# Kernel tuning notes

Hardware: AMD Instinct MI355X
Metric: run time of the kernel (lower is better)

## Reference

```python
import jax, jax.numpy as jnp
import numpy as np

NUM_CAPS = 8
IN_CH = 768
OUT_CH = 64  # == num_routes
BATCH = 16384


def setup_inputs() -> dict:
    key = jax.random.key(0)
    ks = jax.random.split(key, 9)
    lim = 1.0 / np.sqrt(IN_CH)  # torch Linear default init range
    inp = {
        'img_emb': jax.random.normal(ks[0], (BATCH, IN_CH), jnp.float32),
        'capt_emb': jax.random.normal(ks[1], (BATCH, IN_CH), jnp.float32),
        'dct_emb': jax.random.normal(ks[2], (BATCH, IN_CH), jnp.float32),
        'W_img': jax.random.uniform(ks[3], (NUM_CAPS, OUT_CH, IN_CH), jnp.float32, -lim, lim),
        'b_img': jax.random.uniform(ks[4], (NUM_CAPS, OUT_CH), jnp.float32, -lim, lim),
        'W_capt': jax.random.uniform(ks[5], (NUM_CAPS, OUT_CH, IN_CH), jnp.float32, -lim, lim),
        'b_capt': jax.random.uniform(ks[6], (NUM_CAPS, OUT_CH), jnp.float32, -lim, lim),
        'W_dct': jax.random.uniform(ks[7], (NUM_CAPS, OUT_CH, IN_CH), jnp.float32, -lim, lim),
        'b_dct': jax.random.uniform(ks[8], (NUM_CAPS, OUT_CH), jnp.float32, -lim, lim),
    }
    return inp


def _project(x, W, b):
    # x: [B, I]; W: [C, R, I]; b: [C, R] -> [B, R, C]
    # torch: per-capsule Linear y = x @ W_c.T + b_c, viewed [B, R, 1], cat on last dim
    y = jnp.einsum('bi,cri->brc', x, W) + b.T[None]  # [B, R, C]
    return y


def _squash(u, epsilon=1e-07):
    sq = jnp.sum(u * u, axis=-1, keepdims=True)  # [B, 3R, 1]
    safe_norm = jnp.sqrt(sq + epsilon)
    return sq * u / ((1.0 + sq) * safe_norm)


def reference(img_emb, capt_emb, dct_emb, W_img, b_img, W_capt, b_capt, W_dct, b_dct):
    u_img = _project(img_emb, W_img, b_img)      # [B, 64, 8]
    u_capt = _project(capt_emb, W_capt, b_capt)  # [B, 64, 8]
    u_dct = _project(dct_emb, W_dct, b_dct)      # [B, 64, 8]
    combined = jnp.concatenate([u_img, u_capt, u_dct], axis=1)  # [B, 192, 8]
    return _squash(combined)
```

## Files before the change

kernel.cpp:

```cpp
#include <hip/hip_runtime.h>

typedef __attribute__((ext_vector_type(8))) short short8;
typedef __attribute__((ext_vector_type(4))) float floatx4;
typedef __attribute__((ext_vector_type(4))) unsigned int uintx4;

#if __has_builtin(__builtin_amdgcn_cvt_pk_bf16_f32)
typedef __attribute__((ext_vector_type(2))) __bf16 bf16x2;
__device__ __forceinline__ unsigned int pk_bf16(float a, float b) {
  bf16x2 v = __builtin_amdgcn_cvt_pk_bf16_f32(a, b);
  return __builtin_bit_cast(unsigned int, v);
}
#else
__device__ __forceinline__ unsigned int bf16_1(float f) {
  unsigned int u = __builtin_bit_cast(unsigned int, f);
  return (u + 0x7fffu + ((u >> 16) & 1u)) >> 16;
}
__device__ __forceinline__ unsigned int pk_bf16(float a, float b) {
  return bf16_1(a) | (bf16_1(b) << 16);
}
#endif


__global__ __launch_bounds__(256) void prep_w(
    const float* __restrict__ Wi, const float* __restrict__ Wc, const float* __restrict__ Wd,
    const float* __restrict__ bi, const float* __restrict__ bc, const float* __restrict__ bd,
    uintx4* __restrict__ Bprep, float* __restrict__ biasPrep) {
  const int t = blockIdx.x * 256 + threadIdx.x;
  const int l = t & 63;
  const int frag = t >> 6;
  const int nt = frag & 3;
  const int q = frag >> 2;
  const int ks = q % 24;
  const int q2 = q / 24;
  const int h = q2 & 7;
  const int mod = q2 >> 3;
  const int n16 = h * 4 + nt;
  const float* __restrict__ W = (mod == 0) ? Wi : ((mod == 1) ? Wc : Wd);

  const int n = n16 * 16 + (l & 15);
  const int r = n >> 3;
  const int c = n & 7;
  const int i0 = ks * 32 + (l >> 4) * 8;
  const float* src = W + (size_t)(c * 64 + r) * 768 + i0;
  floatx4 f0 = *(const floatx4*)(src);
  floatx4 f1 = *(const floatx4*)(src + 4);
  uintx4 p;
  p.x = pk_bf16(f0.x, f0.y);
  p.y = pk_bf16(f0.z, f0.w);
  p.z = pk_bf16(f1.x, f1.y);
  p.w = pk_bf16(f1.z, f1.w);
  Bprep[(size_t)frag * 64 + l] = p;

  if (t < 1536) {
    const int m2 = t >> 9;
    const int nn = t & 511;
    const float* bb = (m2 == 0) ? bi : ((m2 == 1) ? bc : bd);
    biasPrep[t] = bb[(nn & 7) * 64 + (nn >> 3)];
  }
}

#define LOADA(aa, kk)                                                        \
  {                                                                          \
    _Pragma("unroll") for (int mt = 0; mt < 2; ++mt)                         \
        aa[mt] = Afr[((kk) * 2 + mt) * 64 +                                  \
                     ((ln ^ (((kk) * 4 + quad) & 15)) + (quad << 4))];       \
  }

#define LOADB(bb, kk)                                                        \
  {                                                                          \
    _Pragma("unroll") for (int n2 = 0; n2 < 4; ++n2)                         \
        bb[n2] = bbase[(size_t)((kk) * 4 + n2) * 64];                        \
  }

#define COMP(aa, bb)                                                     \
  {                                                                      \
    _Pragma("unroll") for (int mt = 0; mt < 2; ++mt)                     \
    {                                                                    \
      short8 af = __builtin_bit_cast(short8, aa[mt]);                    \
      _Pragma("unroll") for (int n2 = 0; n2 < 4; ++n2)                   \
          acc[mt][n2] = __builtin_amdgcn_mfma_f32_16x16x32_bf16(         \
              af, __builtin_bit_cast(short8, bb[n2]), acc[mt][n2], 0, 0, \
              0);                                                        \
    }                                                                    \
  }

__global__ __launch_bounds__(512, 4) void caps_fused(
    const float* __restrict__ x0, const float* __restrict__ x1, const float* __restrict__ x2,
    const uintx4* __restrict__ Bprep, const float* __restrict__ biasPrep,
    float* __restrict__ out) {
  __shared__ unsigned long long As64[48 * 128];

  const int tid = threadIdx.x;
  const int bx0 = blockIdx.x;
  const int bx = (bx0 & 7) * 192 + (bx0 >> 3);
  const int mod = bx >> 9;
  const int bm = bx & 511;
  const float* __restrict__ X = (mod == 0) ? x0 : ((mod == 1) ? x1 : x2);

  const float* src = X + (size_t)bm * 32 * 768;
#pragma unroll
  for (int i = 0; i < 12; ++i) {
    const int idx = i * 2048 + tid * 4;
    floatx4 f = *(const floatx4*)(src + idx);
    const int m = (unsigned)idx / 768u;
    const int k = idx - m * 768;
    const int ks = k >> 5;
    const int kk = k & 31;
    const int qk = kk >> 3;
    const int jh = (kk >> 2) & 1;
    const int mt = m >> 4;
    const int lnn = m & 15;
    const int p = (ks * 4 + qk) & 15;
    const int slot = (lnn ^ p) + (qk << 4);
    unsigned long long w =
        ((unsigned long long)pk_bf16(f.z, f.w) << 32) | pk_bf16(f.x, f.y);
    As64[(((ks * 2 + mt) * 64 + slot) << 1) + jh] = w;
  }
  __syncthreads();

  const int lane = tid & 63;
  const int ln = lane & 15;
  const int quad = lane >> 4;
  const int wv = tid >> 6;

  const uintx4* Afr = (const uintx4*)As64;
  const uintx4* bbase = Bprep + (size_t)(mod * 8 + wv) * (96 * 64) + lane;

  floatx4 acc[2][4] = {};
  uintx4 a0[2], a1[2], b0[4], b1[4];

  LOADA(a0, 0);
  LOADB(b0, 0);
#pragma unroll 1
  for (int ks2 = 0; ks2 < 12; ++ks2) {
    const int ks = 2 * ks2;
    LOADA(a1, ks + 1);
    LOADB(b1, ks + 1);
    COMP(a0, b0);
    if (ks2 != 11) {
      LOADA(a0, ks + 2);
      LOADB(b0, ks + 2);
    }
    COMP(a1, b1);
  }

  const int col0 = mod * 512 + wv * 64 + ln;
  float bias[4];
#pragma unroll
  for (int n2 = 0; n2 < 4; ++n2) bias[n2] = biasPrep[col0 + n2 * 16];

#pragma unroll
  for (int mt = 0; mt < 2; ++mt) {
    const size_t rbase = (size_t)(bm * 32 + mt * 16 + quad * 4) * 1536;
#pragma unroll
    for (int n2 = 0; n2 < 4; ++n2) {
      float* op = out + rbase + col0 + n2 * 16;
#pragma unroll
      for (int jj = 0; jj < 4; ++jj) {
        float u = acc[mt][n2][jj] + bias[n2];
        float s = u * u;
        s += __shfl_xor(s, 1);
        s += __shfl_xor(s, 2);
        s += __shfl_xor(s, 4);
#if __has_builtin(__builtin_amdgcn_rsqf) && __has_builtin(__builtin_amdgcn_rcpf)
        float sc = s * __builtin_amdgcn_rsqf(s + 1e-7f) *
                   __builtin_amdgcn_rcpf(1.0f + s);
#else
        float sc = s / ((1.0f + s) * sqrtf(s + 1e-7f));
#endif
        op[(size_t)jj * 1536] = u * sc;
      }
    }
  }
}

extern "C" void kernel_launch(void* const* d_in, const int* in_sizes, int n_in,
                              void* d_out, int out_size, void* d_ws, size_t ws_size,
                              hipStream_t stream) {
  const float* ximg = (const float*)d_in[0];
  const float* xcapt = (const float*)d_in[1];
  const float* xdct = (const float*)d_in[2];
  const float* Wi = (const float*)d_in[3];
  const float* bi = (const float*)d_in[4];
  const float* Wc = (const float*)d_in[5];
  const float* bc = (const float*)d_in[6];
  const float* Wd = (const float*)d_in[7];
  const float* bd = (const float*)d_in[8];

  uintx4* Bprep = (uintx4*)d_ws;
  float* biasPrep = (float*)((char*)d_ws + 2304 * 1024);

  hipLaunchKernelGGL(prep_w, dim3(576), dim3(256), 0, stream,
                     Wi, Wc, Wd, bi, bc, bd, Bprep, biasPrep);
  hipLaunchKernelGGL(caps_fused, dim3(1536), dim3(512), 0, stream,
                     ximg, xcapt, xdct, (const uintx4*)Bprep, biasPrep,
                     (float*)d_out);
}
```

Measured before the change: 82.36 us.

## Double row tile per block to 64 rows with 1024 threads and K-split staging

Each block now handles 64 rows instead of 32, using 16 waves arranged as 2 row-groups by 8 column-groups, so each weight fragment loaded from global memory serves twice as many rows. To fit the larger A tile in the same shared-memory buffer, the K dimension is staged in two halves of 384, with extra barriers between the halves. The grid halves to 768 blocks. This cuts weight traffic per output row but serializes the second half's staging behind compute, and a 1024-thread block limits occupancy and flexibility.

```diff
diff --git a/kernel.cpp b/kernel.cpp
--- a/kernel.cpp
+++ b/kernel.cpp
@@ -59,14 +59,35 @@
   }
 }
 
-#define LOADA(aa, kk)                                                        \
+#define STAGE(p)                                                             \
+  {                                                                          \
+    _Pragma("unroll") for (int i = 0; i < 6; ++i) {                          \
+      const int idx = i * 4096 + tid * 4;           \
+      const int m = (unsigned)idx / 384u;                                    \
+      const int k = idx - m * 384;                                           \
+      floatx4 f = *(const floatx4*)(srcbase + (size_t)m * 768 + (p)*384 + k);\
+      const int ks = k >> 5;                         \
+      const int kk = k & 31;                                                 \
+      const int qk = kk >> 3;                                                \
+      const int jh = (kk >> 2) & 1;                                          \
+      const int mtg = m >> 4;                         \
+      const int lnn = m & 15;                                                \
+      const int px = (ks * 4 + qk) & 15;                \
+      const int slot = (lnn ^ px) + (qk << 4);                               \
+      unsigned long long w =                                                 \
+          ((unsigned long long)pk_bf16(f.z, f.w) << 32) | pk_bf16(f.x, f.y); \
+      As64[(((ks * 4 + mtg) * 64 + slot) << 1) + jh] = w;                    \
+    }                                                                        \
+  }
+
+#define LOADA(aa, kk)                           \
   {                                                                          \
     _Pragma("unroll") for (int mt = 0; mt < 2; ++mt)                         \
-        aa[mt] = Afr[((kk) * 2 + mt) * 64 +                                  \
+        aa[mt] = Afr[((kk) * 4 + wr2 + mt) * 64 +                            \
                      ((ln ^ (((kk) * 4 + quad) & 15)) + (quad << 4))];       \
   }
 
-#define LOADB(bb, kk)                                                        \
+#define LOADB(bb, kk)                          \
   {                                                                          \
     _Pragma("unroll") for (int n2 = 0; n2 < 4; ++n2)                         \
         bb[n2] = bbase[(size_t)((kk) * 4 + n2) * 64];                        \
@@ -84,7 +105,7 @@
     }                                                                    \
   }
 
-__global__ __launch_bounds__(512, 4) void caps_fused(
+__global__ __launch_bounds__(1024, 4) void caps_fused(
     const float* __restrict__ x0, const float* __restrict__ x1, const float* __restrict__ x2,
     const uintx4* __restrict__ Bprep, const float* __restrict__ biasPrep,
     float* __restrict__ out) {
@@ -92,66 +113,60 @@
 
   const int tid = threadIdx.x;
   const int bx0 = blockIdx.x;
-  const int bx = (bx0 & 7) * 192 + (bx0 >> 3);
-  const int mod = bx >> 9;
-  const int bm = bx & 511;
+  const int bx = (bx0 & 7) * 96 + (bx0 >> 3);
+  const int mod = bx >> 8;
+  const int bm = bx & 255;
   const float* __restrict__ X = (mod == 0) ? x0 : ((mod == 1) ? x1 : x2);
-
-  const float* src = X + (size_t)bm * 32 * 768;
-#pragma unroll
-  for (int i = 0; i < 12; ++i) {
-    const int idx = i * 2048 + tid * 4;
-    floatx4 f = *(const floatx4*)(src + idx);
-    const int m = (unsigned)idx / 768u;
-    const int k = idx - m * 768;
-    const int ks = k >> 5;
-    const int kk = k & 31;
-    const int qk = kk >> 3;
-    const int jh = (kk >> 2) & 1;
-    const int mt = m >> 4;
-    const int lnn = m & 15;
-    const int p = (ks * 4 + qk) & 15;
-    const int slot = (lnn ^ p) + (qk << 4);
-    unsigned long long w =
-        ((unsigned long long)pk_bf16(f.z, f.w) << 32) | pk_bf16(f.x, f.y);
-    As64[(((ks * 2 + mt) * 64 + slot) << 1) + jh] = w;
-  }
-  __syncthreads();
+  const float* srcbase = X + (size_t)bm * 64 * 768;
 
   const int lane = tid & 63;
   const int ln = lane & 15;
   const int quad = lane >> 4;
   const int wv = tid >> 6;
+  const int wr = wv >> 3;
+  const int wc = wv & 7;
+  const int wr2 = wr << 1;
 
   const uintx4* Afr = (const uintx4*)As64;
-  const uintx4* bbase = Bprep + (size_t)(mod * 8 + wv) * (96 * 64) + lane;
+  const uintx4* bbase = Bprep + (size_t)(mod * 8 + wc) * (96 * 64) + lane;
 
   floatx4 acc[2][4] = {};
   uintx4 a0[2], a1[2], b0[4], b1[4];
 
+  STAGE(0);
+  __syncthreads();
   LOADA(a0, 0);
   LOADB(b0, 0);
 #pragma unroll 1
-  for (int ks2 = 0; ks2 < 12; ++ks2) {
-    const int ks = 2 * ks2;
-    LOADA(a1, ks + 1);
-    LOADB(b1, ks + 1);
+  for (int it = 0; it < 6; ++it) {
+    const int s = 2 * it;
+    LOADA(a1, s + 1); LOADB(b1, s + 1);
     COMP(a0, b0);
-    if (ks2 != 11) {
-      LOADA(a0, ks + 2);
-      LOADB(b0, ks + 2);
-    }
+    if (it != 5) { LOADA(a0, s + 2); LOADB(b0, s + 2); }
     COMP(a1, b1);
   }
-
-  const int col0 = mod * 512 + wv * 64 + ln;
+  LOADB(b0, 12);
+  __syncthreads();
+  STAGE(1);
+  __syncthreads();
+  LOADA(a0, 0);
+#pragma unroll 1
+  for (int it = 0; it < 6; ++it) {
+    const int s = 2 * it;
+    LOADA(a1, s + 1); LOADB(b1, 12 + s + 1);
+    COMP(a0, b0);
+    if (it != 5) { LOADA(a0, s + 2); LOADB(b0, 12 + s + 2); }
+    COMP(a1, b1);
+  }
+
+  const int col0 = mod * 512 + wc * 64 + ln;
   float bias[4];
 #pragma unroll
   for (int n2 = 0; n2 < 4; ++n2) bias[n2] = biasPrep[col0 + n2 * 16];
 
 #pragma unroll
   for (int mt = 0; mt < 2; ++mt) {
-    const size_t rbase = (size_t)(bm * 32 + mt * 16 + quad * 4) * 1536;
+    const size_t rbase = (size_t)(bm * 64 + wr * 32 + mt * 16 + quad * 4) * 1536;
 #pragma unroll
     for (int n2 = 0; n2 < 4; ++n2) {
       float* op = out + rbase + col0 + n2 * 16;
@@ -192,7 +207,7 @@
 
   hipLaunchKernelGGL(prep_w, dim3(576), dim3(256), 0, stream,
                      Wi, Wc, Wd, bi, bc, bd, Bprep, biasPrep);
-  hipLaunchKernelGGL(caps_fused, dim3(1536), dim3(512), 0, stream,
+  hipLaunchKernelGGL(caps_fused, dim3(768), dim3(1024), 0, stream,
                      ximg, xcapt, xdct, (const uintx4*)Bprep, biasPrep,
                      (float*)d_out);
 }
```

Measured after the change: 90.50 us. 9.9% more time.
